# Performance work log

Hardware: AMD Instinct MI355X
Metric: run time of the kernel (lower is better)

## Reference

```python
import jax, jax.numpy as jnp
import numpy as np

L = 3        # number of GatedGCN layers
N = 30000    # nodes
E = 480000   # edges (avg degree 16)
D = 128      # hidden dim (= in_dim = out_dim)
IN = 128     # input feature dim
G = 64       # graphs in batch
C = 10       # classes


def setup_inputs() -> dict:
    key = jax.random.key(0)
    ks = jax.random.split(key, 32)
    s = 0.05  # weight scale to keep activations / sigmoid gates in a sane range
    inp = {
        "h": jax.random.normal(ks[0], (N, IN), jnp.float32),
        "e": jax.random.normal(ks[1], (E, IN), jnp.float32),
        "snorm_n": jax.random.uniform(ks[2], (N, 1), jnp.float32),
        "snorm_e": jax.random.uniform(ks[3], (E, 1), jnp.float32),
        "src": jax.random.randint(ks[4], (E,), 0, N, jnp.int32),
        "dst": jax.random.randint(ks[5], (E,), 0, N, jnp.int32),
        "graph_id": jnp.sort(jax.random.randint(ks[6], (N,), 0, G, jnp.int32)),
        # input embeddings
        "Wh_emb": jax.random.normal(ks[7], (IN, D), jnp.float32) * s,
        "bh_emb": jnp.zeros((D,), jnp.float32),
        "We_emb": jax.random.normal(ks[8], (IN, D), jnp.float32) * s,
        "be_emb": jnp.zeros((D,), jnp.float32),
        # per-layer A,B,C,D,E linears (stacked over L)
        "WA": jax.random.normal(ks[9], (L, D, D), jnp.float32) * s,
        "bA": jnp.zeros((L, D), jnp.float32),
        "WB": jax.random.normal(ks[10], (L, D, D), jnp.float32) * s,
        "bB": jnp.zeros((L, D), jnp.float32),
        "WC": jax.random.normal(ks[11], (L, D, D), jnp.float32) * s,
        "bC": jnp.zeros((L, D), jnp.float32),
        "WD": jax.random.normal(ks[12], (L, D, D), jnp.float32) * s,
        "bD": jnp.zeros((L, D), jnp.float32),
        "WE": jax.random.normal(ks[13], (L, D, D), jnp.float32) * s,
        "bE": jnp.zeros((L, D), jnp.float32),
        # batch-norm affine params (node / edge)
        "gn_h": jnp.ones((L, D), jnp.float32),
        "bt_h": jnp.zeros((L, D), jnp.float32),
        "gn_e": jnp.ones((L, D), jnp.float32),
        "bt_e": jnp.zeros((L, D), jnp.float32),
        # readout linear
        "Wr": jax.random.normal(ks[14], (D, C), jnp.float32) * s,
        "br": jnp.zeros((C,), jnp.float32),
    }
    return inp


def _bn(x, gamma, beta):
    # training-mode BatchNorm1d: biased batch stats over the node/edge axis
    mu = jnp.mean(x, axis=0)
    var = jnp.var(x, axis=0)
    return (x - mu) * jax.lax.rsqrt(var + 1e-5) * gamma + beta


def reference(h, e, snorm_n, snorm_e, src, dst, graph_id,
              Wh_emb, bh_emb, We_emb, be_emb,
              WA, bA, WB, bB, WC, bC, WD, bD, WE, bE,
              gn_h, bt_h, gn_e, bt_e, Wr, br):
    n_nodes = h.shape[0]
    h = h @ Wh_emb + bh_emb
    e = e @ We_emb + be_emb
    for l in range(WA.shape[0]):
        h_in, e_in = h, e
        Ah = h @ WA[l] + bA[l]
        Bh = h @ WB[l] + bB[l]
        Dh = h @ WD[l] + bD[l]
        Eh = h @ WE[l] + bE[l]
        Ce = e @ WC[l] + bC[l]
        # message: e_ij = Ce + Dh_src + Eh_dst ; gate = sigmoid(e_ij)
        e_new = Ce + Dh[src] + Eh[dst]                       # [E, D]
        sig = jax.nn.sigmoid(e_new)
        # reduce at dst: gated weighted mean of Bh_src
        num = jax.ops.segment_sum(sig * Bh[src], dst, num_segments=n_nodes)
        den = jax.ops.segment_sum(sig, dst, num_segments=n_nodes)
        h_new = Ah + num / (den + 1e-6)
        # graph norm
        h_new = h_new * snorm_n
        e_new = e_new * snorm_e
        # batch norm + ReLU + residual (dropout p=0 -> identity)
        h_new = jax.nn.relu(_bn(h_new, gn_h[l], bt_h[l]))
        e_new = jax.nn.relu(_bn(e_new, gn_e[l], bt_e[l]))
        h = h_in + h_new
        e = e_in + e_new
    # mean_nodes readout per graph, then linear classifier
    sums = jax.ops.segment_sum(h, graph_id, num_segments=G)
    cnt = jax.ops.segment_sum(jnp.ones((n_nodes, 1), h.dtype), graph_id, num_segments=G)
    hg = sums / jnp.maximum(cnt, 1.0)
    return hg @ Wr + br
```

## Files before the change

### kernel.cpp

```cpp
#include <hip/hip_runtime.h>
#include <cstdint>
#include <cstddef>

#define N_NODES  30000
#define N_EDGES  480000
#define N_LAYERS 3
#define N_GRAPHS 64
#define N_CLASS  10
#define NREP     32

typedef __attribute__((ext_vector_type(8))) short short8v;
typedef __attribute__((ext_vector_type(4))) float f32x4;

__device__ __forceinline__ unsigned short f2bf(float x) {
  union { float f; unsigned u; } v; v.f = x;
  unsigned r = v.u + 0x7FFFu + ((v.u >> 16) & 1u);
  return (unsigned short)(r >> 16);
}
__device__ __forceinline__ float bf2f(unsigned short h) {
  union { unsigned u; float f; } v; v.u = ((unsigned)h) << 16;
  return v.f;
}
__device__ __forceinline__ int swzW(int row, int off16) {
  return (row << 8) | (off16 ^ ((row & 7) << 4));
}

__global__ void wconv(const float* __restrict__ Wh, const float* __restrict__ We,
                      const float* __restrict__ WA, const float* __restrict__ WB,
                      const float* __restrict__ WC, const float* __restrict__ WD,
                      const float* __restrict__ WE, unsigned short* __restrict__ Wt)
{
  const int mi  = blockIdx.x >> 6;
  const int idx = (blockIdx.x & 63) * 256 + threadIdx.x;
  const float* src;
  if      (mi == 0) src = Wh;
  else if (mi == 1) src = We;
  else if (mi < 5)  src = WA + (size_t)(mi - 2) * 16384;
  else if (mi < 8)  src = WB + (size_t)(mi - 5) * 16384;
  else if (mi < 11) src = WC + (size_t)(mi - 8) * 16384;
  else if (mi < 14) src = WD + (size_t)(mi - 11) * 16384;
  else              src = WE + (size_t)(mi - 14) * 16384;
  const int k = idx >> 7, n = idx & 127;
  Wt[(size_t)mi * 16384 + (size_t)n * 128 + k] = f2bf(src[idx]);
}

struct GemmArgs {
  const unsigned short* Wt[4];
  const float* bias[4];
  unsigned short* out[4];
};

template<int NMAT, int AMODE>
__global__ __launch_bounds__(256)
void gemm_mm(const void* __restrict__ Ap, GemmArgs g, int M,
             const unsigned short* __restrict__ tb, const float2* __restrict__ pqh,
             unsigned short* __restrict__ hout,
             const unsigned short* __restrict__ WtX, const float* __restrict__ biasX)
{
  __shared__ __align__(16) unsigned char WL[32768];
  unsigned short* Wl = (unsigned short*)WL;
  const int t = threadIdx.x;
  const int w = t >> 6, l = t & 63;
  const int lr = l & 15, lkb = (l >> 4) * 8;
  const int r0 = blockIdx.x * 64;
  const bool vrow = (r0 + w * 16 + lr) < M;
  int arow = r0 + w * 16 + lr; if (arow >= M) arow = M - 1;

  short8v a[4];
  if (AMODE == 2) {
#pragma unroll
    for (int p = 0; p < 8; ++p) {
      const int ci = t + p * 256;
      *(short8v*)(WL + swzW(ci >> 4, (ci & 15) * 16)) = *(const short8v*)(WtX + (size_t)ci * 8);
    }
    const float* A = (const float*)Ap;
#pragma unroll
    for (int kk = 0; kk < 4; ++kk) {
      const float* p = A + (size_t)arow * 128 + kk * 32 + lkb;
      const float4 u = *(const float4*)p;
      const float4 v = *(const float4*)(p + 4);
      short8v av;
      av[0]=f2bf(u.x); av[1]=f2bf(u.y); av[2]=f2bf(u.z); av[3]=f2bf(u.w);
      av[4]=f2bf(v.x); av[5]=f2bf(v.y); av[6]=f2bf(v.z); av[7]=f2bf(v.w);
      a[kk] = av;
    }
    __syncthreads();
    f32x4 acc[8];
#pragma unroll
    for (int ct = 0; ct < 8; ++ct) acc[ct] = (f32x4){0.f, 0.f, 0.f, 0.f};
#pragma unroll
    for (int kk = 0; kk < 4; ++kk)
#pragma unroll
      for (int ct = 0; ct < 8; ++ct) {
        const short8v b = *(const short8v*)(WL + swzW(ct * 16 + lr, kk * 64 + (l >> 4) * 16));
        acc[ct] = __builtin_amdgcn_mfma_f32_16x16x32_bf16(a[kk], b, acc[ct], 0, 0, 0);
      }
    __syncthreads();
#pragma unroll
    for (int ct = 0; ct < 8; ++ct) {
      const float bb = biasX[ct * 16 + lr];
#pragma unroll
      for (int q = 0; q < 4; ++q)
        Wl[(w * 16 + (l >> 4) * 4 + q) * 136 + ct * 16 + lr] = f2bf(acc[ct][q] + bb);
    }
    __syncthreads();
#pragma unroll
    for (int kk = 0; kk < 4; ++kk) {
      a[kk] = *(const short8v*)(Wl + (w * 16 + lr) * 136 + kk * 32 + lkb);
      if (vrow) *(short8v*)(hout + (size_t)arow * 128 + kk * 32 + lkb) = a[kk];
    }
  } else if (AMODE == 1) {
    const unsigned short* A = (const unsigned short*)Ap;
#pragma unroll
    for (int kk = 0; kk < 4; ++kk) {
      const short8v tv = *(const short8v*)(tb + (size_t)arow * 128 + kk * 32 + lkb);
      const short8v hr = *(const short8v*)(A + (size_t)arow * 128 + kk * 32 + lkb);
      short8v av;
#pragma unroll
      for (int j = 0; j < 8; ++j) {
        const float2 PQ = pqh[kk * 32 + lkb + j];
        const float x = bf2f((unsigned short)tv[j]) * PQ.x + PQ.y;
        av[j] = (short)f2bf(bf2f((unsigned short)hr[j]) + fmaxf(x, 0.f));
      }
      a[kk] = av;
      if (vrow) *(short8v*)(hout + (size_t)arow * 128 + kk * 32 + lkb) = av;
    }
  } else {
    const unsigned short* A = (const unsigned short*)Ap;
#pragma unroll
    for (int kk = 0; kk < 4; ++kk)
      a[kk] = *(const short8v*)(A + (size_t)arow * 128 + kk * 32 + lkb);
  }

#pragma unroll
  for (int m = 0; m < NMAT; ++m) {
    if (m || AMODE == 2) __syncthreads();
#pragma unroll
    for (int p = 0; p < 8; ++p) {
      const int ci = t + p * 256;
      *(short8v*)(WL + swzW(ci >> 4, (ci & 15) * 16)) = *(const short8v*)(g.Wt[m] + (size_t)ci * 8);
    }
    __syncthreads();
    f32x4 acc[8];
#pragma unroll
    for (int ct = 0; ct < 8; ++ct) acc[ct] = (f32x4){0.f, 0.f, 0.f, 0.f};
#pragma unroll
    for (int kk = 0; kk < 4; ++kk)
#pragma unroll
      for (int ct = 0; ct < 8; ++ct) {
        const short8v b = *(const short8v*)(WL + swzW(ct * 16 + lr, kk * 64 + (l >> 4) * 16));
        acc[ct] = __builtin_amdgcn_mfma_f32_16x16x32_bf16(a[kk], b, acc[ct], 0, 0, 0);
      }
    __syncthreads();
#pragma unroll
    for (int ct = 0; ct < 8; ++ct) {
      const float bb = g.bias[m][ct * 16 + lr];
#pragma unroll
      for (int q = 0; q < 4; ++q)
        Wl[(w * 16 + (l >> 4) * 4 + q) * 136 + ct * 16 + lr] = f2bf(acc[ct][q] + bb);
    }
    __syncthreads();
    unsigned short* out = g.out[m];
#pragma unroll
    for (int p = 0; p < 4; ++p) {
      const int ci = t + p * 256;
      const int rr = ci >> 4, co = (ci & 15) * 8;
      const int grow = r0 + rr;
      if (grow < M)
        *(short8v*)(out + (size_t)grow * 128 + co) = *(const short8v*)(Wl + rr * 136 + co);
    }
  }
}

template<int LMODE>
__global__ __launch_bounds__(256)
void edge_kern(const float* __restrict__ e_in, const int* __restrict__ csr,
               unsigned short* __restrict__ eres, unsigned short* __restrict__ enew,
               const unsigned short* __restrict__ WtEmb, const float* __restrict__ bEmb,
               const unsigned short* __restrict__ WtC, const float* __restrict__ bC,
               const unsigned short* __restrict__ Dh, const unsigned short* __restrict__ Eh,
               const int* __restrict__ csrc, const int* __restrict__ cdst,
               const float* __restrict__ csne, const float2* __restrict__ pq)
{
  extern __shared__ __align__(16) char smem[];
  char* SM = smem;
  unsigned short* TB = (unsigned short*)((LMODE == 0) ? (smem + 32768) : smem);
  const int t = threadIdx.x;
  const int w = t >> 6, l = t & 63;
  const int lr = l & 15, lkb = (l >> 4) * 8;
  const int r0 = blockIdx.x * 64;
  const int pos = r0 + w * 16 + lr;

  short8v a[4];
  f32x4 acc[8];
  short8v dpre[4], epre[4];

  if (LMODE == 0) {
#pragma unroll
    for (int p = 0; p < 8; ++p) {
      const int ci = t + p * 256;
      *(short8v*)(SM + swzW(ci >> 4, (ci & 15) * 16)) = *(const short8v*)(WtEmb + (size_t)ci * 8);
    }
#pragma unroll
    for (int p = 0; p < 4; ++p) {
      const int ci = t + p * 256;
      const int rr = ci >> 4, co = (ci & 15) * 8;
      const float* sp = e_in + (size_t)csr[r0 + rr] * 128 + co;
      const float4 u = *(const float4*)sp;
      const float4 v = *(const float4*)(sp + 4);
      short8v av;
      av[0]=f2bf(u.x); av[1]=f2bf(u.y); av[2]=f2bf(u.z); av[3]=f2bf(u.w);
      av[4]=f2bf(v.x); av[5]=f2bf(v.y); av[6]=f2bf(v.z); av[7]=f2bf(v.w);
      *(short8v*)(TB + rr * 132 + co) = av;
    }
    __syncthreads();
#pragma unroll
    for (int kk = 0; kk < 4; ++kk)
      a[kk] = *(const short8v*)(TB + (w * 16 + lr) * 132 + kk * 32 + lkb);
#pragma unroll
    for (int ct = 0; ct < 8; ++ct) acc[ct] = (f32x4){0.f, 0.f, 0.f, 0.f};
#pragma unroll
    for (int kk = 0; kk < 4; ++kk)
#pragma unroll
      for (int ct = 0; ct < 8; ++ct) {
        const short8v b = *(const short8v*)(SM + swzW(ct * 16 + lr, kk * 64 + (l >> 4) * 16));
        acc[ct] = __builtin_amdgcn_mfma_f32_16x16x32_bf16(a[kk], b, acc[ct], 0, 0, 0);
      }
    __syncthreads();
#pragma unroll
    for (int ct = 0; ct < 8; ++ct) {
      const float bb = bEmb[ct * 16 + lr];
#pragma unroll
      for (int q = 0; q < 4; ++q)
        TB[(w * 16 + (l >> 4) * 4 + q) * 132 + ct * 16 + lr] = f2bf(acc[ct][q] + bb);
    }
#pragma unroll
    for (int p = 0; p < 8; ++p) {
      const int ci = t + p * 256;
      *(short8v*)(SM + swzW(ci >> 4, (ci & 15) * 16)) = *(const short8v*)(WtC + (size_t)ci * 8);
    }
    __syncthreads();
#pragma unroll
    for (int kk = 0; kk < 4; ++kk) {
      a[kk] = *(const short8v*)(TB + (w * 16 + lr) * 132 + kk * 32 + lkb);
      *(short8v*)(eres + (size_t)pos * 128 + kk * 32 + lkb) = a[kk];
    }
  } else {
#pragma unroll
    for (int p = 0; p < 8; ++p) {
      const int ci = t + p * 256;
      *(short8v*)(SM + swzW(ci >> 4, (ci & 15) * 16)) = *(const short8v*)(WtC + (size_t)ci * 8);
    }
    const float sn = csne[pos];
    short8v ep[4], er[4];
#pragma unroll
    for (int kk = 0; kk < 4; ++kk) {
      ep[kk] = *(const short8v*)(enew + (size_t)pos * 128 + kk * 32 + lkb);
      er[kk] = *(const short8v*)(eres + (size_t)pos * 128 + kk * 32 + lkb);
    }
#pragma unroll
    for (int kk = 0; kk < 4; ++kk) {
      short8v av;
#pragma unroll
      for (int j = 0; j < 8; ++j) {
        const float2 PQ = pq[kk * 32 + lkb + j];
        const float x = bf2f((unsigned short)ep[kk][j]) * sn * PQ.x + PQ.y;
        av[j] = (short)f2bf(bf2f((unsigned short)er[kk][j]) + fmaxf(x, 0.f));
      }
      a[kk] = av;
      if (LMODE == 2)
        *(short8v*)(eres + (size_t)pos * 128 + kk * 32 + lkb) = av;
    }
    __syncthreads();
  }

#pragma unroll
  for (int p = 0; p < 4; ++p) {
    const int ci = t + p * 256;
    const int rr = ci >> 4, co = (ci & 15) * 8;
    const int pp = r0 + rr;
    dpre[p] = *(const short8v*)(Dh + (size_t)csrc[pp] * 128 + co);
    epre[p] = *(const short8v*)(Eh + (size_t)cdst[pp] * 128 + co);
  }

#pragma unroll
  for (int ct = 0; ct < 8; ++ct) acc[ct] = (f32x4){0.f, 0.f, 0.f, 0.f};
#pragma unroll
  for (int kk = 0; kk < 4; ++kk)
#pragma unroll
    for (int ct = 0; ct < 8; ++ct) {
      const short8v b = *(const short8v*)(SM + swzW(ct * 16 + lr, kk * 64 + (l >> 4) * 16));
      acc[ct] = __builtin_amdgcn_mfma_f32_16x16x32_bf16(a[kk], b, acc[ct], 0, 0, 0);
    }
  __syncthreads();
#pragma unroll
  for (int ct = 0; ct < 8; ++ct) {
    const float bb = bC[ct * 16 + lr];
#pragma unroll
    for (int q = 0; q < 4; ++q)
      TB[(w * 16 + (l >> 4) * 4 + q) * 132 + ct * 16 + lr] = f2bf(acc[ct][q] + bb);
  }
  __syncthreads();
#pragma unroll
  for (int p = 0; p < 4; ++p) {
    const int ci = t + p * 256;
    const int rr = ci >> 4, co = (ci & 15) * 8;
    const int pp = r0 + rr;
    const short8v ce = *(const short8v*)(TB + rr * 132 + co);
    short8v ov;
#pragma unroll
    for (int j = 0; j < 8; ++j)
      ov[j] = (short)f2bf(bf2f((unsigned short)ce[j]) + bf2f((unsigned short)dpre[p][j]) + bf2f((unsigned short)epre[p][j]));
    *(short8v*)(enew + (size_t)pp * 128 + co) = ov;
  }
}

__global__ void hist_kernel(const int* __restrict__ dst, int* __restrict__ cnt, int E)
{
  const int i = blockIdx.x * 256 + threadIdx.x;
  if (i < E) atomicAdd(&cnt[dst[i]], 1);
}

__global__ void scan_kernel(const int* __restrict__ cnt, int* __restrict__ start,
                            int* __restrict__ cursor, int n, int total)
{
  __shared__ int lds[1024];
  const int tid = threadIdx.x;
  const int chunk = (n + 1023) / 1024;
  const int lo = tid * chunk, hi = min(lo + chunk, n);
  int s = 0;
  for (int i = lo; i < hi; ++i) s += cnt[i];
  lds[tid] = s;
  __syncthreads();
  for (int off = 1; off < 1024; off <<= 1) {
    const int v = (tid >= off) ? lds[tid - off] : 0;
    __syncthreads();
    lds[tid] += v;
    __syncthreads();
  }
  int run = (tid == 0) ? 0 : lds[tid - 1];
  for (int i = lo; i < hi; ++i) { start[i] = run; cursor[i] = run; run += cnt[i]; }
  if (tid == 0) start[n] = total;
}

__global__ void scatter_kernel(const int* __restrict__ dst, const int* __restrict__ src,
                               const float* __restrict__ sne, int* __restrict__ cursor,
                               int* __restrict__ csr, int* __restrict__ csrc,
                               int* __restrict__ cdst, float* __restrict__ csne, int E)
{
  const int i = blockIdx.x * 256 + threadIdx.x;
  if (i < E) {
    const int p = atomicAdd(&cursor[dst[i]], 1);
    csr[p] = i; csrc[p] = src[i]; cdst[p] = dst[i]; csne[p] = sne[i];
  }
}

template<int DOE>
__global__ __launch_bounds__(256)
void aggregate(const unsigned short* __restrict__ enew, const unsigned short* __restrict__ Bh,
               const unsigned short* __restrict__ Ah, const float* __restrict__ snorm_n,
               const int* __restrict__ start, const int* __restrict__ csrc,
               const float* __restrict__ csne,
               unsigned short* __restrict__ tbuf, float* __restrict__ statrep)
{
  __shared__ float2 red[16][132];
  const int t = threadIdx.x;
  const int g = t >> 4, q = t & 15;
  const int v = blockIdx.x * 16 + g;
  const int s0 = start[v], s1 = start[v + 1];
  float num[8] = {0,0,0,0,0,0,0,0}, den[8] = {0,0,0,0,0,0,0,0};
  float psE[8] = {0,0,0,0,0,0,0,0}, pqE[8] = {0,0,0,0,0,0,0,0};

  float sn = 0.f;
  short8v ev = {}, bv = {};
  if (s0 < s1) {
    if (DOE) sn = csne[s0];
    ev = *(const short8v*)(enew + (size_t)s0 * 128 + q * 8);
    bv = *(const short8v*)(Bh + (size_t)csrc[s0] * 128 + q * 8);
  }
  for (int i = s0; i < s1; ++i) {
    float snn = 0.f;
    short8v evn = {}, bvn = {};
    if (i + 1 < s1) {
      if (DOE) snn = csne[i + 1];
      evn = *(const short8v*)(enew + (size_t)(i + 1) * 128 + q * 8);
      bvn = *(const short8v*)(Bh + (size_t)csrc[i + 1] * 128 + q * 8);
    }
#pragma unroll
    for (int j = 0; j < 8; ++j) {
      const float en = bf2f((unsigned short)ev[j]);
      const float sg = 1.f / (1.f + __expf(-en));
      num[j] = fmaf(sg, bf2f((unsigned short)bv[j]), num[j]);
      den[j] += sg;
      if (DOE) { const float tv = en * sn; psE[j] += tv; pqE[j] = fmaf(tv, tv, pqE[j]); }
    }
    ev = evn; bv = bvn; sn = snn;
  }
  const float snv = snorm_n[v];
  const short8v av = *(const short8v*)(Ah + (size_t)v * 128 + q * 8);
  float hv[8];
  short8v tout;
#pragma unroll
  for (int j = 0; j < 8; ++j) {
    hv[j] = (bf2f((unsigned short)av[j]) + num[j] / (den[j] + 1e-6f)) * snv;
    tout[j] = (short)f2bf(hv[j]);
  }
  *(short8v*)(tbuf + (size_t)v * 128 + q * 8) = tout;

  float* rep = statrep + (size_t)(blockIdx.x & (NREP - 1)) * 512;
#pragma unroll
  for (int j = 0; j < 8; ++j) red[g][q * 8 + j] = make_float2(hv[j], hv[j] * hv[j]);
  __syncthreads();
  if (t < 128) {
    float s = 0.f, qq = 0.f;
    for (int gg = 0; gg < 16; ++gg) { s += red[gg][t].x; qq += red[gg][t].y; }
    atomicAdd(rep + t, s); atomicAdd(rep + 128 + t, qq);
  }
  if (DOE) {
    __syncthreads();
#pragma unroll
    for (int j = 0; j < 8; ++j) red[g][q * 8 + j] = make_float2(psE[j], pqE[j]);
    __syncthreads();
    if (t < 128) {
      float s = 0.f, qq = 0.f;
      for (int gg = 0; gg < 16; ++gg) { s += red[gg][t].x; qq += red[gg][t].y; }
      atomicAdd(rep + 256 + t, s); atomicAdd(rep + 384 + t, qq);
    }
  }
}

__global__ void finalize_kernel(float* __restrict__ rep, float2* __restrict__ pqh,
                                float2* __restrict__ pqe,
                                const float* __restrict__ gn_h_l, const float* __restrict__ bt_h_l,
                                const float* __restrict__ gn_e_l, const float* __restrict__ bt_e_l,
                                float invN, float invE, int doE)
{
  const int c = threadIdx.x;
  float sH = 0.f, qH = 0.f, sE = 0.f, qE = 0.f;
  for (int r = 0; r < NREP; ++r) {
    float* p = rep + (size_t)r * 512;
    sH += p[c]; qH += p[128 + c]; sE += p[256 + c]; qE += p[384 + c];
    p[c] = 0.f; p[128 + c] = 0.f; p[256 + c] = 0.f; p[384 + c] = 0.f;
  }
  const float muH = sH * invN;
  const float vH  = fmaxf(qH * invN - muH * muH, 0.f);
  const float PH  = rsqrtf(vH + 1e-5f) * gn_h_l[c];
  pqh[c] = make_float2(PH, bt_h_l[c] - muH * PH);
  if (doE) {
    const float muE = sE * invE;
    const float vE  = fmaxf(qE * invE - muE * muE, 0.f);
    const float PE  = rsqrtf(vE + 1e-5f) * gn_e_l[c];
    pqe[c] = make_float2(PE, bt_e_l[c] - muE * PE);
  }
}

__global__ void readout_scatter(const unsigned short* __restrict__ h, const unsigned short* __restrict__ tb,
                                const float2* __restrict__ pqh, const int* __restrict__ gid,
                                float* __restrict__ gsum, int* __restrict__ gcnt, int N)
{
  const int c = threadIdx.x;
  const float2 PQ = pqh[c];
  const int row0 = blockIdx.x * 256;
  int cur = -1, cnt = 0;
  float s = 0.f;
  for (int r = 0; r < 256; ++r) {
    const int v = row0 + r;
    if (v >= N) break;
    const int g = gid[v];
    if (g != cur) {
      if (cur >= 0) {
        atomicAdd(&gsum[(size_t)cur * 128 + c], s);
        if (c == 0) atomicAdd(&gcnt[cur], cnt);
      }
      cur = g; s = 0.f; cnt = 0;
    }
    s += bf2f(h[(size_t)v * 128 + c]) + fmaxf(bf2f(tb[(size_t)v * 128 + c]) * PQ.x + PQ.y, 0.f);
    ++cnt;
  }
  if (cur >= 0) {
    atomicAdd(&gsum[(size_t)cur * 128 + c], s);
    if (c == 0) atomicAdd(&gcnt[cur], cnt);
  }
}

__global__ void readout_final(const float* __restrict__ gsum, const int* __restrict__ gcnt,
                              const float* __restrict__ Wr, const float* __restrict__ br,
                              float* __restrict__ out)
{
  const int g = blockIdx.x;
  const int t = threadIdx.x;
  __shared__ float hg[128];
  const float cnt = fmaxf((float)gcnt[g], 1.f);
  hg[t] = gsum[(size_t)g * 128 + t] / cnt;
  __syncthreads();
  if (t < N_CLASS) {
    float acc = br[t];
    for (int k = 0; k < 128; ++k) acc = fmaf(hg[k], Wr[k * N_CLASS + t], acc);
    out[g * N_CLASS + t] = acc;
  }
}

extern "C" void kernel_launch(void* const* d_in, const int* in_sizes, int n_in,
                              void* d_out, int out_size, void* d_ws, size_t ws_size,
                              hipStream_t stream)
{
  const float* h_in    = (const float*)d_in[0];
  const float* e_in    = (const float*)d_in[1];
  const float* snorm_n = (const float*)d_in[2];
  const float* snorm_e = (const float*)d_in[3];
  const int*   src     = (const int*)d_in[4];
  const int*   dst     = (const int*)d_in[5];
  const int*   gid     = (const int*)d_in[6];
  const float* Wh_emb  = (const float*)d_in[7];
  const float* bh_emb  = (const float*)d_in[8];
  const float* We_emb  = (const float*)d_in[9];
  const float* be_emb  = (const float*)d_in[10];
  const float* WA = (const float*)d_in[11]; const float* bA = (const float*)d_in[12];
  const float* WB = (const float*)d_in[13]; const float* bB = (const float*)d_in[14];
  const float* WC = (const float*)d_in[15]; const float* bC = (const float*)d_in[16];
  const float* WD = (const float*)d_in[17]; const float* bD = (const float*)d_in[18];
  const float* WE = (const float*)d_in[19]; const float* bE = (const float*)d_in[20];
  const float* gn_h = (const float*)d_in[21]; const float* bt_h = (const float*)d_in[22];
  const float* gn_e = (const float*)d_in[23]; const float* bt_e = (const float*)d_in[24];
  const float* Wr = (const float*)d_in[25]; const float* br = (const float*)d_in[26];
  float* out = (float*)d_out;
  (void)in_sizes; (void)n_in; (void)out_size; (void)ws_size;

  char* ws = (char*)d_ws;
  size_t off = 0;
  auto alloc = [&](size_t bytes) -> char* {
    off = (off + 255) & ~(size_t)255;
    char* p = ws + off;
    off += bytes;
    return p;
  };
  const size_t ND = (size_t)N_NODES * 128, ED = (size_t)N_EDGES * 128;
  unsigned short* hbuf = (unsigned short*)alloc(ND * 2);
  unsigned short* ebuf = (unsigned short*)alloc(ED * 2);
  unsigned short* enew = (unsigned short*)alloc(ED * 2);
  unsigned short* Ah   = (unsigned short*)alloc(ND * 2);
  unsigned short* Bh   = (unsigned short*)alloc(ND * 2);
  unsigned short* Dh   = (unsigned short*)alloc(ND * 2);
  unsigned short* Eh   = (unsigned short*)alloc(ND * 2);
  unsigned short* tbuf = (unsigned short*)alloc(ND * 2);
  unsigned short* Wt   = (unsigned short*)alloc((size_t)17 * 16384 * 2);
  float2* pqh          = (float2*)alloc(128 * 8);
  float2* pqe          = (float2*)alloc(128 * 8);
  int* start  = (int*)alloc((size_t)(N_NODES + 1) * 4);
  int* cursor = (int*)alloc((size_t)N_NODES * 4);
  int* csr    = (int*)alloc((size_t)N_EDGES * 4);
  int* csrc   = (int*)alloc((size_t)N_EDGES * 4);
  int* cdst   = (int*)alloc((size_t)N_EDGES * 4);
  float* csne = (float*)alloc((size_t)N_EDGES * 4);
  char* zbase = (char*)alloc(0);
  int*   cnt     = (int*)alloc((size_t)N_NODES * 4);
  float* statrep = (float*)alloc((size_t)NREP * 512 * 4);
  float* gsum    = (float*)alloc((size_t)N_GRAPHS * 128 * 4);
  int*   gcnt    = (int*)alloc((size_t)N_GRAPHS * 4);
  char* zend = (char*)alloc(0);

  hipMemsetAsync(zbase, 0, (size_t)(zend - zbase), stream);

  wconv<<<17 * 64, 256, 0, stream>>>(Wh_emb, We_emb, WA, WB, WC, WD, WE, Wt);

  hist_kernel<<<(N_EDGES + 255) / 256, 256, 0, stream>>>(dst, cnt, N_EDGES);
  scan_kernel<<<1, 1024, 0, stream>>>(cnt, start, cursor, N_NODES, N_EDGES);
  scatter_kernel<<<(N_EDGES + 255) / 256, 256, 0, stream>>>(dst, src, snorm_e, cursor,
                                                            csr, csrc, cdst, csne, N_EDGES);

  const int gbN = (N_NODES + 63) / 64;
  const int gbE = N_EDGES / 64;
  const unsigned SH0 = 49664;
  const unsigned SH2 = 32768;

  for (int l = 0; l < N_LAYERS; ++l) {
    const size_t bOff = (size_t)l * 128;
    const int doE = (l < N_LAYERS - 1) ? 1 : 0;
    {
      GemmArgs g{};
      g.Wt[0] = Wt + (size_t)(2 + l)  * 16384; g.bias[0] = bA + bOff; g.out[0] = Ah;
      g.Wt[1] = Wt + (size_t)(5 + l)  * 16384; g.bias[1] = bB + bOff; g.out[1] = Bh;
      g.Wt[2] = Wt + (size_t)(11 + l) * 16384; g.bias[2] = bD + bOff; g.out[2] = Dh;
      g.Wt[3] = Wt + (size_t)(14 + l) * 16384; g.bias[3] = bE + bOff; g.out[3] = Eh;
      if (l == 0)
        gemm_mm<4, 2><<<gbN, 256, 0, stream>>>(h_in, g, N_NODES, nullptr, nullptr, hbuf,
                                               Wt + 0 * 16384, bh_emb);
      else
        gemm_mm<4, 1><<<gbN, 256, 0, stream>>>(hbuf, g, N_NODES, tbuf, pqh, hbuf,
                                               nullptr, nullptr);
    }
    const unsigned short* WtC = Wt + (size_t)(8 + l) * 16384;
    if (l == 0)
      edge_kern<0><<<gbE, 256, SH0, stream>>>(e_in, csr, ebuf, enew, Wt + 1 * 16384, be_emb,
                                              WtC, bC + bOff, Dh, Eh, csrc, cdst, csne, nullptr);
    else if (l == 1)
      edge_kern<2><<<gbE, 256, SH2, stream>>>(nullptr, nullptr, ebuf, enew, nullptr, nullptr,
                                              WtC, bC + bOff, Dh, Eh, csrc, cdst, csne, pqe);
    else
      edge_kern<3><<<gbE, 256, SH2, stream>>>(nullptr, nullptr, ebuf, enew, nullptr, nullptr,
                                              WtC, bC + bOff, Dh, Eh, csrc, cdst, csne, pqe);
    if (doE)
      aggregate<1><<<N_NODES / 16, 256, 0, stream>>>(enew, Bh, Ah, snorm_n, start, csrc, csne,
                                                     tbuf, statrep);
    else
      aggregate<0><<<N_NODES / 16, 256, 0, stream>>>(enew, Bh, Ah, snorm_n, start, csrc, csne,
                                                     tbuf, statrep);
    finalize_kernel<<<1, 128, 0, stream>>>(statrep, pqh, pqe, gn_h + bOff, bt_h + bOff,
                                           gn_e + bOff, bt_e + bOff,
                                           1.f / N_NODES, 1.f / N_EDGES, doE);
  }

  readout_scatter<<<(N_NODES + 255) / 256, 128, 0, stream>>>(hbuf, tbuf, pqh, gid, gsum, gcnt, N_NODES);
  readout_final<<<N_GRAPHS, 128, 0, stream>>>(gsum, gcnt, Wr, br, out);
}
```

Measured before the change: 904.9 us.

## Split node GEMM across two grid rows and parallelize aggregation over edges

The node GEMM now runs with a 2D grid where each blockIdx.y computes two of the four output matrices, doubling block count, and the in-place residual update becomes ping-pong buffers so the input h is not overwritten while the other half still reads it. The aggregate kernel assigns one wavefront per node, with four 16-lane groups striding over incoming edges and combining partials via shuffles, instead of 16 lanes per node. This targets low occupancy and serial per-node edge loops, at the cost of recomputing the A-operand prologue twice and issuing more blocks with more atomics.

Measured after the change: 866.7 us (median of 2 runs). -4.2%, faster.

```diff
diff --git a/kernel.cpp b/kernel.cpp
--- a/kernel.cpp
+++ b/kernel.cpp
@@ -60,6 +60,8 @@
   __shared__ __align__(16) unsigned char WL[32768];
   unsigned short* Wl = (unsigned short*)WL;
   const int t = threadIdx.x;
+  const int mbase = blockIdx.y * NMAT;
+  const bool wr0 = (blockIdx.y == 0);
   const int w = t >> 6, l = t & 63;
   const int lr = l & 15, lkb = (l >> 4) * 8;
   const int r0 = blockIdx.x * 64;
@@ -107,7 +109,7 @@
 #pragma unroll
     for (int kk = 0; kk < 4; ++kk) {
       a[kk] = *(const short8v*)(Wl + (w * 16 + lr) * 136 + kk * 32 + lkb);
-      if (vrow) *(short8v*)(hout + (size_t)arow * 128 + kk * 32 + lkb) = a[kk];
+      if (wr0 && vrow) *(short8v*)(hout + (size_t)arow * 128 + kk * 32 + lkb) = a[kk];
     }
   } else if (AMODE == 1) {
     const unsigned short* A = (const unsigned short*)Ap;
@@ -123,7 +125,7 @@
         av[j] = (short)f2bf(bf2f((unsigned short)hr[j]) + fmaxf(x, 0.f));
       }
       a[kk] = av;
-      if (vrow) *(short8v*)(hout + (size_t)arow * 128 + kk * 32 + lkb) = av;
+      if (wr0 && vrow) *(short8v*)(hout + (size_t)arow * 128 + kk * 32 + lkb) = av;
     }
   } else {
     const unsigned short* A = (const unsigned short*)Ap;
@@ -138,7 +140,7 @@
 #pragma unroll
     for (int p = 0; p < 8; ++p) {
       const int ci = t + p * 256;
-      *(short8v*)(WL + swzW(ci >> 4, (ci & 15) * 16)) = *(const short8v*)(g.Wt[m] + (size_t)ci * 8);
+      *(short8v*)(WL + swzW(ci >> 4, (ci & 15) * 16)) = *(const short8v*)(g.Wt[mbase + m] + (size_t)ci * 8);
     }
     __syncthreads();
     f32x4 acc[8];
@@ -154,13 +156,13 @@
     __syncthreads();
 #pragma unroll
     for (int ct = 0; ct < 8; ++ct) {
-      const float bb = g.bias[m][ct * 16 + lr];
+      const float bb = g.bias[mbase + m][ct * 16 + lr];
 #pragma unroll
       for (int q = 0; q < 4; ++q)
         Wl[(w * 16 + (l >> 4) * 4 + q) * 136 + ct * 16 + lr] = f2bf(acc[ct][q] + bb);
     }
     __syncthreads();
-    unsigned short* out = g.out[m];
+    unsigned short* out = g.out[mbase + m];
 #pragma unroll
     for (int p = 0; p < 4; ++p) {
       const int ci = t + p * 256;
@@ -363,28 +365,33 @@
                const float* __restrict__ csne,
                unsigned short* __restrict__ tbuf, float* __restrict__ statrep)
 {
-  __shared__ float2 red[16][132];
+  __shared__ float2 red[4][132];
+  __shared__ float2 redE[4][132];
   const int t = threadIdx.x;
-  const int g = t >> 4, q = t & 15;
-  const int v = blockIdx.x * 16 + g;
+  const int wv = t >> 6;
+  const int lane = t & 63;
+  const int sub = lane >> 4;
+  const int q = lane & 15;
+  const int v = blockIdx.x * 4 + wv;
   const int s0 = start[v], s1 = start[v + 1];
   float num[8] = {0,0,0,0,0,0,0,0}, den[8] = {0,0,0,0,0,0,0,0};
   float psE[8] = {0,0,0,0,0,0,0,0}, pqE[8] = {0,0,0,0,0,0,0,0};
 
+  int i = s0 + sub;
   float sn = 0.f;
   short8v ev = {}, bv = {};
-  if (s0 < s1) {
-    if (DOE) sn = csne[s0];
-    ev = *(const short8v*)(enew + (size_t)s0 * 128 + q * 8);
-    bv = *(const short8v*)(Bh + (size_t)csrc[s0] * 128 + q * 8);
-  }
-  for (int i = s0; i < s1; ++i) {
+  if (i < s1) {
+    if (DOE) sn = csne[i];
+    ev = *(const short8v*)(enew + (size_t)i * 128 + q * 8);
+    bv = *(const short8v*)(Bh + (size_t)csrc[i] * 128 + q * 8);
+  }
+  for (; i < s1; i += 4) {
     float snn = 0.f;
     short8v evn = {}, bvn = {};
-    if (i + 1 < s1) {
-      if (DOE) snn = csne[i + 1];
-      evn = *(const short8v*)(enew + (size_t)(i + 1) * 128 + q * 8);
-      bvn = *(const short8v*)(Bh + (size_t)csrc[i + 1] * 128 + q * 8);
+    if (i + 4 < s1) {
+      if (DOE) snn = csne[i + 4];
+      evn = *(const short8v*)(enew + (size_t)(i + 4) * 128 + q * 8);
+      bvn = *(const short8v*)(Bh + (size_t)csrc[i + 4] * 128 + q * 8);
     }
 #pragma unroll
     for (int j = 0; j < 8; ++j) {
@@ -396,35 +403,44 @@
     }
     ev = evn; bv = bvn; sn = snn;
   }
-  const float snv = snorm_n[v];
-  const short8v av = *(const short8v*)(Ah + (size_t)v * 128 + q * 8);
-  float hv[8];
-  short8v tout;
 #pragma unroll
   for (int j = 0; j < 8; ++j) {
-    hv[j] = (bf2f((unsigned short)av[j]) + num[j] / (den[j] + 1e-6f)) * snv;
-    tout[j] = (short)f2bf(hv[j]);
-  }
-  *(short8v*)(tbuf + (size_t)v * 128 + q * 8) = tout;
-
+    num[j] += __shfl_xor(num[j], 16, 64);
+    num[j] += __shfl_xor(num[j], 32, 64);
+    den[j] += __shfl_xor(den[j], 16, 64);
+    den[j] += __shfl_xor(den[j], 32, 64);
+    if (DOE) {
+      psE[j] += __shfl_xor(psE[j], 16, 64);
+      psE[j] += __shfl_xor(psE[j], 32, 64);
+      pqE[j] += __shfl_xor(pqE[j], 16, 64);
+      pqE[j] += __shfl_xor(pqE[j], 32, 64);
+    }
+  }
+  if (sub == 0) {
+    const float snv = snorm_n[v];
+    const short8v av = *(const short8v*)(Ah + (size_t)v * 128 + q * 8);
+    short8v tout;
+#pragma unroll
+    for (int j = 0; j < 8; ++j) {
+      const float hv = (bf2f((unsigned short)av[j]) + num[j] / (den[j] + 1e-6f)) * snv;
+      tout[j] = (short)f2bf(hv);
+      red[wv][q * 8 + j] = make_float2(hv, hv * hv);
+      if (DOE) redE[wv][q * 8 + j] = make_float2(psE[j], pqE[j]);
+    }
+    *(short8v*)(tbuf + (size_t)v * 128 + q * 8) = tout;
+  }
+  __syncthreads();
   float* rep = statrep + (size_t)(blockIdx.x & (NREP - 1)) * 512;
-#pragma unroll
-  for (int j = 0; j < 8; ++j) red[g][q * 8 + j] = make_float2(hv[j], hv[j] * hv[j]);
-  __syncthreads();
   if (t < 128) {
     float s = 0.f, qq = 0.f;
-    for (int gg = 0; gg < 16; ++gg) { s += red[gg][t].x; qq += red[gg][t].y; }
+#pragma unroll
+    for (int gg = 0; gg < 4; ++gg) { s += red[gg][t].x; qq += red[gg][t].y; }
     atomicAdd(rep + t, s); atomicAdd(rep + 128 + t, qq);
-  }
-  if (DOE) {
-    __syncthreads();
-#pragma unroll
-    for (int j = 0; j < 8; ++j) red[g][q * 8 + j] = make_float2(psE[j], pqE[j]);
-    __syncthreads();
-    if (t < 128) {
-      float s = 0.f, qq = 0.f;
-      for (int gg = 0; gg < 16; ++gg) { s += red[gg][t].x; qq += red[gg][t].y; }
-      atomicAdd(rep + 256 + t, s); atomicAdd(rep + 384 + t, qq);
+    if (DOE) {
+      float se = 0.f, qe = 0.f;
+#pragma unroll
+      for (int gg = 0; gg < 4; ++gg) { se += redE[gg][t].x; qe += redE[gg][t].y; }
+      atomicAdd(rep + 256 + t, se); atomicAdd(rep + 384 + t, qe);
     }
   }
 }
@@ -535,9 +551,10 @@
     return p;
   };
   const size_t ND = (size_t)N_NODES * 128, ED = (size_t)N_EDGES * 128;
-  unsigned short* hbuf = (unsigned short*)alloc(ND * 2);
-  unsigned short* ebuf = (unsigned short*)alloc(ED * 2);
-  unsigned short* enew = (unsigned short*)alloc(ED * 2);
+  unsigned short* hbufA = (unsigned short*)alloc(ND * 2);
+  unsigned short* hbufB = (unsigned short*)alloc(ND * 2);
+  unsigned short* ebuf  = (unsigned short*)alloc(ED * 2);
+  unsigned short* enew  = (unsigned short*)alloc(ED * 2);
   unsigned short* Ah   = (unsigned short*)alloc(ND * 2);
   unsigned short* Bh   = (unsigned short*)alloc(ND * 2);
   unsigned short* Dh   = (unsigned short*)alloc(ND * 2);
@@ -570,8 +587,12 @@
 
   const int gbN = (N_NODES + 63) / 64;
   const int gbE = N_EDGES / 64;
+  const dim3 gN(gbN, 2);
   const unsigned SH0 = 49664;
   const unsigned SH2 = 32768;
+
+  unsigned short* hcur = hbufA;
+  unsigned short* hnxt = hbufB;
 
   for (int l = 0; l < N_LAYERS; ++l) {
     const size_t bOff = (size_t)l * 128;
@@ -582,12 +603,14 @@
       g.Wt[1] = Wt + (size_t)(5 + l)  * 16384; g.bias[1] = bB + bOff; g.out[1] = Bh;
       g.Wt[2] = Wt + (size_t)(11 + l) * 16384; g.bias[2] = bD + bOff; g.out[2] = Dh;
       g.Wt[3] = Wt + (size_t)(14 + l) * 16384; g.bias[3] = bE + bOff; g.out[3] = Eh;
-      if (l == 0)
-        gemm_mm<4, 2><<<gbN, 256, 0, stream>>>(h_in, g, N_NODES, nullptr, nullptr, hbuf,
-                                               Wt + 0 * 16384, bh_emb);
-      else
-        gemm_mm<4, 1><<<gbN, 256, 0, stream>>>(hbuf, g, N_NODES, tbuf, pqh, hbuf,
-                                               nullptr, nullptr);
+      if (l == 0) {
+        gemm_mm<2, 2><<<gN, 256, 0, stream>>>(h_in, g, N_NODES, nullptr, nullptr, hcur,
+                                              Wt + 0 * 16384, bh_emb);
+      } else {
+        gemm_mm<2, 1><<<gN, 256, 0, stream>>>(hcur, g, N_NODES, tbuf, pqh, hnxt,
+                                              nullptr, nullptr);
+        unsigned short* tmp = hcur; hcur = hnxt; hnxt = tmp;
+      }
     }
     const unsigned short* WtC = Wt + (size_t)(8 + l) * 16384;
     if (l == 0)
@@ -600,16 +623,16 @@
       edge_kern<3><<<gbE, 256, SH2, stream>>>(nullptr, nullptr, ebuf, enew, nullptr, nullptr,
                                               WtC, bC + bOff, Dh, Eh, csrc, cdst, csne, pqe);
     if (doE)
-      aggregate<1><<<N_NODES / 16, 256, 0, stream>>>(enew, Bh, Ah, snorm_n, start, csrc, csne,
-                                                     tbuf, statrep);
+      aggregate<1><<<N_NODES / 4, 256, 0, stream>>>(enew, Bh, Ah, snorm_n, start, csrc, csne,
+                                                    tbuf, statrep);
     else
-      aggregate<0><<<N_NODES / 16, 256, 0, stream>>>(enew, Bh, Ah, snorm_n, start, csrc, csne,
-                                                     tbuf, statrep);
+      aggregate<0><<<N_NODES / 4, 256, 0, stream>>>(enew, Bh, Ah, snorm_n, start, csrc, csne,
+                                                    tbuf, statrep);
     finalize_kernel<<<1, 128, 0, stream>>>(statrep, pqh, pqe, gn_h + bOff, bt_h + bOff,
                                            gn_e + bOff, bt_e + bOff,
                                            1.f / N_NODES, 1.f / N_EDGES, doE);
   }
 
-  readout_scatter<<<(N_NODES + 255) / 256, 128, 0, stream>>>(hbuf, tbuf, pqh, gid, gsum, gcnt, N_NODES);
+  readout_scatter<<<(N_NODES + 255) / 256, 128, 0, stream>>>(hcur, tbuf, pqh, gid, gsum, gcnt, N_NODES);
   readout_final<<<N_GRAPHS, 128, 0, stream>>>(gsum, gcnt, Wr, br, out);
 }
```
